# Optimization experiments

Hardware: AMD Instinct MI355X
Metric: run time of the kernel (lower is better)

The kernel has to match this reference:

```python
import jax, jax.numpy as jnp
import numpy as np

IN_FEATURES = 4096
OUT_FEATURES = 8192
LUT_SIZE = 65536  # 256 * 256 two-level codebook


def setup_inputs() -> dict:
    key = jax.random.key(0)
    k_x, k_b, k_f, k_s, k_l = jax.random.split(key, 5)
    x = jax.random.normal(k_x, (2, 256, IN_FEATURES), dtype=jnp.float32)
    base_idx = jax.random.randint(k_b, (OUT_FEATURES, IN_FEATURES), 0, 256, dtype=jnp.int32)
    fine_idx = jax.random.randint(k_f, (OUT_FEATURES, IN_FEATURES), 0, 256, dtype=jnp.int32)
    scale = jax.random.uniform(k_s, (OUT_FEATURES, 1), dtype=jnp.float32)
    lut = jax.random.normal(k_l, (LUT_SIZE,), dtype=jnp.float32)
    return {"x": x, "base_idx": base_idx, "fine_idx": fine_idx, "scale": scale, "lut": lut}


def reference(x, base_idx, fine_idx, scale, lut):
    # Two-level LUT dequant: combined 16-bit index = base*256 + fine
    combined_idx = base_idx * 256 + fine_idx              # [out, in] int32
    weights = lut[combined_idx] * scale                   # [out, in] fp32, per-row scale
    # F.linear(x, weights) == x @ weights.T
    return jnp.einsum('bsi,oi->bso', x, weights)
```

## Files before the change

### kernel.cpp

```cpp
#include <hip/hip_runtime.h>

typedef unsigned short ushort_t;
typedef unsigned int   uint32;
typedef __attribute__((ext_vector_type(8)))  short short8;
typedef __attribute__((ext_vector_type(4)))  float floatx4;
typedef __attribute__((ext_vector_type(16))) float floatx16;

#define IN_F   4096
#define OUT_F  8192
#define M_TOT  512

__device__ __forceinline__ ushort_t f2bf(float f) {
    uint32 u = __builtin_bit_cast(uint32, f);
    u += 0x7FFFu + ((u >> 16) & 1u);
    return (ushort_t)(u >> 16);
}

__global__ void cvt_x_kernel(const float* __restrict__ x, ushort_t* __restrict__ xb) {
    int i = (blockIdx.x * 256 + threadIdx.x) * 8;
    float4 v0 = *(const float4*)(x + i);
    float4 v1 = *(const float4*)(x + i + 4);
    short8 s;
    s[0] = (short)f2bf(v0.x); s[1] = (short)f2bf(v0.y);
    s[2] = (short)f2bf(v0.z); s[3] = (short)f2bf(v0.w);
    s[4] = (short)f2bf(v1.x); s[5] = (short)f2bf(v1.y);
    s[6] = (short)f2bf(v1.z); s[7] = (short)f2bf(v1.w);
    *(short8*)(xb + i) = s;
}

__global__ __launch_bounds__(1024, 4)
void dequant_kernel(const int* __restrict__ base_idx, const int* __restrict__ fine_idx,
                    const float* __restrict__ lut, ushort_t* __restrict__ wq)
{
    __shared__ ushort_t sh_lut[65536];
    const int tid = threadIdx.x;
    for (int i = tid * 4; i < 65536; i += 1024 * 4) {
        float4 v = *(const float4*)(lut + i);
        sh_lut[i + 0] = f2bf(v.x);
        sh_lut[i + 1] = f2bf(v.y);
        sh_lut[i + 2] = f2bf(v.z);
        sh_lut[i + 3] = f2bf(v.w);
    }
    __syncthreads();

    const int row = blockIdx.x * 32 + (tid >> 5);
    const int k0  = (tid & 31) * 4;
    const int* bp = base_idx + (size_t)row * IN_F + k0;
    const int* fp = fine_idx + (size_t)row * IN_F + k0;
    ushort_t*  op = wq       + (size_t)row * IN_F + k0;

    int4 cb[4], cf[4];
#pragma unroll
    for (int u = 0; u < 4; ++u) {
        cb[u] = *(const int4*)(bp + u * 128);
        cf[u] = *(const int4*)(fp + u * 128);
    }
    for (int b = 0; b < 8; ++b) {
        int4 nb[4], nf[4];
        const int bn = (b + 1 < 8) ? b + 1 : b;
#pragma unroll
        for (int u = 0; u < 4; ++u) {
            nb[u] = *(const int4*)(bp + (bn * 4 + u) * 128);
            nf[u] = *(const int4*)(fp + (bn * 4 + u) * 128);
        }
#pragma unroll
        for (int u = 0; u < 4; ++u) {
            uint32 w0 = (uint32)sh_lut[(cb[u].x << 8) + cf[u].x]
                      | ((uint32)sh_lut[(cb[u].y << 8) + cf[u].y] << 16);
            uint32 w1 = (uint32)sh_lut[(cb[u].z << 8) + cf[u].z]
                      | ((uint32)sh_lut[(cb[u].w << 8) + cf[u].w] << 16);
            uint2 wv; wv.x = w0; wv.y = w1;
            *(uint2*)(op + (size_t)(b * 4 + u) * 128) = wv;
        }
#pragma unroll
        for (int u = 0; u < 4; ++u) { cb[u] = nb[u]; cf[u] = nf[u]; }
    }
}

#define BK 128
__global__ __launch_bounds__(256)
void gemm_kernel(const ushort_t* __restrict__ xb, const ushort_t* __restrict__ wq,
                 const float* __restrict__ scale, float* __restrict__ out)
{
    __shared__ ushort_t shA[128 * BK];
    __shared__ ushort_t shB[128 * BK];

    const int tid  = threadIdx.x;
    const int wave = tid >> 6;
    const int m0   = blockIdx.x * 128;
    const int n0   = blockIdx.y * 128;

    const int g = (tid & 15) ^ ((tid >> 4) & 7);
    const ushort_t* aBase = xb + (size_t)(m0 + (tid >> 4)) * IN_F + g * 8;
    const ushort_t* bBase = wq + (size_t)(n0 + (tid >> 4)) * IN_F + g * 8;
    typedef __attribute__((address_space(3))) ushort_t lds_us;
    typedef const __attribute__((address_space(1))) void gvoid;
    lds_us* sA3 = (lds_us*)shA;
    lds_us* sB3 = (lds_us*)shB;

    const int lane = tid & 63;
    const int l31  = lane & 31;
    const int lhi  = lane >> 5;
    const int qm   = wave & 1;
    const int qn   = wave >> 1;
    const int rx   = l31 & 7;

    floatx16 acc[2][2];
    const floatx16 z16 = {0.f,0.f,0.f,0.f,0.f,0.f,0.f,0.f,0.f,0.f,0.f,0.f,0.f,0.f,0.f,0.f};
    acc[0][0] = z16; acc[0][1] = z16; acc[1][0] = z16; acc[1][1] = z16;

    for (int kb = 0; kb < IN_F; kb += BK) {
#pragma unroll
        for (int i = 0; i < 8; ++i) {
            __builtin_amdgcn_global_load_lds((gvoid*)(aBase + (size_t)i * 16 * IN_F + kb),
                (__attribute__((address_space(3))) void*)(sA3 + i * 2048 + wave * 512),
                16, 0, 0);
            __builtin_amdgcn_global_load_lds((gvoid*)(bBase + (size_t)i * 16 * IN_F + kb),
                (__attribute__((address_space(3))) void*)(sB3 + i * 2048 + wave * 512),
                16, 0, 0);
        }
        __syncthreads();

#pragma unroll
        for (int ks = 0; ks < 8; ++ks) {
            const int p = ((2 * ks + lhi) ^ rx) * 8;
            short8 a0 = *(const short8*)&shA[(qm * 64 +      l31) * BK + p];
            short8 a1 = *(const short8*)&shA[(qm * 64 + 32 + l31) * BK + p];
            short8 b0 = *(const short8*)&shB[(qn * 64 +      l31) * BK + p];
            short8 b1 = *(const short8*)&shB[(qn * 64 + 32 + l31) * BK + p];
            acc[0][0] = __builtin_amdgcn_mfma_f32_32x32x16_bf16(a0, b0, acc[0][0], 0, 0, 0);
            acc[0][1] = __builtin_amdgcn_mfma_f32_32x32x16_bf16(a0, b1, acc[0][1], 0, 0, 0);
            acc[1][0] = __builtin_amdgcn_mfma_f32_32x32x16_bf16(a1, b0, acc[1][0], 0, 0, 0);
            acc[1][1] = __builtin_amdgcn_mfma_f32_32x32x16_bf16(a1, b1, acc[1][1], 0, 0, 0);
        }
        __syncthreads();
    }

#pragma unroll
    for (int nt = 0; nt < 2; ++nt) {
        const int col = n0 + qn * 64 + nt * 32 + l31;
        const float sc = scale[col];
#pragma unroll
        for (int mt = 0; mt < 2; ++mt) {
            const int rbase = m0 + qm * 64 + mt * 32 + 4 * lhi;
#pragma unroll
            for (int reg = 0; reg < 16; ++reg) {
                const int row = rbase + (reg & 3) + 8 * (reg >> 2);
                out[(size_t)row * OUT_F + col] = acc[mt][nt][reg] * sc;
            }
        }
    }
}

#define NB  32
#define FBK 128
#define WS  136
#define NITER (IN_F / FBK)
template<bool XBF16>
__global__ __launch_bounds__(1024, 4)
void ghost_kernel(const float* __restrict__ xf, const ushort_t* __restrict__ xb,
                  const int* __restrict__ base_idx, const int* __restrict__ fine_idx,
                  const float* __restrict__ scale, const float* __restrict__ lut,
                  float* __restrict__ out)
{
    __shared__ ushort_t sh_lut[65536];
    __shared__ ushort_t sh_w[2][NB * WS];
    const int tid = threadIdx.x;
    const int n0  = blockIdx.x * NB;
    for (int i = tid * 4; i < 65536; i += 1024 * 4) {
        float4 v = *(const float4*)(lut + i);
        sh_lut[i + 0] = f2bf(v.x); sh_lut[i + 1] = f2bf(v.y);
        sh_lut[i + 2] = f2bf(v.z); sh_lut[i + 3] = f2bf(v.w);
    }
    const int sn  = tid >> 5;
    const int skq = (tid & 31) * 4;
    const int* bp = base_idx + (size_t)(n0 + sn) * IN_F + skq;
    const int* fp = fine_idx + (size_t)(n0 + sn) * IN_F + skq;
    __syncthreads();
    int4 pb = *(const int4*)(bp);
    int4 pf = *(const int4*)(fp);
    {
        uint32 w0 = (uint32)sh_lut[(pb.x << 8) + pf.x] | ((uint32)sh_lut[(pb.y << 8) + pf.y] << 16);
        uint32 w1 = (uint32)sh_lut[(pb.z << 8) + pf.z] | ((uint32)sh_lut[(pb.w << 8) + pf.w] << 16);
        uint2 wv; wv.x = w0; wv.y = w1;
        *(uint2*)&sh_w[0][sn * WS + skq] = wv;
    }
    pb = *(const int4*)(bp + FBK);
    pf = *(const int4*)(fp + FBK);
    __syncthreads();
    const int lane = tid & 63;
    const int wave = tid >> 6;
    const int l16  = lane & 15;
    const int quad = lane >> 4;
    floatx4 acc[2][2];
    const floatx4 zero = {0.f, 0.f, 0.f, 0.f};
    acc[0][0] = zero; acc[0][1] = zero; acc[1][0] = zero; acc[1][1] = zero;
    const int mrow = wave * 32 + l16;
    const ushort_t* xrow  = XBF16 ? (xb + (size_t)mrow * IN_F + quad * 8) : (const ushort_t*)nullptr;
    const float*    xrowf = XBF16 ? (const float*)nullptr : (xf + (size_t)mrow * IN_F + quad * 8);
    for (int t = 0; t < NITER; ++t) {
        const int k0 = t * FBK;
        {
            uint32 w0 = (uint32)sh_lut[(pb.x << 8) + pf.x] | ((uint32)sh_lut[(pb.y << 8) + pf.y] << 16);
            uint32 w1 = (uint32)sh_lut[(pb.z << 8) + pf.z] | ((uint32)sh_lut[(pb.w << 8) + pf.w] << 16);
            uint2 wv; wv.x = w0; wv.y = w1;
            *(uint2*)&sh_w[(t + 1) & 1][sn * WS + skq] = wv;
        }
        {
            const int kk = (t + 2 < NITER ? t + 2 : NITER - 1) * FBK;
            pb = *(const int4*)(bp + kk);
            pf = *(const int4*)(fp + kk);
        }
        const ushort_t* wb = sh_w[t & 1];
#pragma unroll
        for (int ks = 0; ks < 4; ++ks) {
            const int kk = k0 + ks * 32;
            short8 b0 = *(const short8*)&wb[l16        * WS + ks * 32 + quad * 8];
            short8 b1 = *(const short8*)&wb[(16 + l16) * WS + ks * 32 + quad * 8];
            short8 a0, a1;
            if (XBF16) {
                a0 = *(const short8*)(xrow + kk);
                a1 = *(const short8*)(xrow + (size_t)16 * IN_F + kk);
            } else {
                const float* p0 = xrowf + kk;
                const float* p1 = xrowf + (size_t)16 * IN_F + kk;
                float4 u0 = *(const float4*)p0, u1 = *(const float4*)(p0 + 4);
                float4 v0 = *(const float4*)p1, v1 = *(const float4*)(p1 + 4);
                a0[0] = (short)f2bf(u0.x); a0[1] = (short)f2bf(u0.y);
                a0[2] = (short)f2bf(u0.z); a0[3] = (short)f2bf(u0.w);
                a0[4] = (short)f2bf(u1.x); a0[5] = (short)f2bf(u1.y);
                a0[6] = (short)f2bf(u1.z); a0[7] = (short)f2bf(u1.w);
                a1[0] = (short)f2bf(v0.x); a1[1] = (short)f2bf(v0.y);
                a1[2] = (short)f2bf(v0.z); a1[3] = (short)f2bf(v0.w);
                a1[4] = (short)f2bf(v1.x); a1[5] = (short)f2bf(v1.y);
                a1[6] = (short)f2bf(v1.z); a1[7] = (short)f2bf(v1.w);
            }
            acc[0][0] = __builtin_amdgcn_mfma_f32_16x16x32_bf16(a0, b0, acc[0][0], 0, 0, 0);
            acc[0][1] = __builtin_amdgcn_mfma_f32_16x16x32_bf16(a0, b1, acc[0][1], 0, 0, 0);
            acc[1][0] = __builtin_amdgcn_mfma_f32_16x16x32_bf16(a1, b0, acc[1][0], 0, 0, 0);
            acc[1][1] = __builtin_amdgcn_mfma_f32_16x16x32_bf16(a1, b1, acc[1][1], 0, 0, 0);
        }
        __syncthreads();
    }
#pragma unroll
    for (int nf = 0; nf < 2; ++nf) {
        const int col = n0 + nf * 16 + l16;
        const float sc = scale[col];
#pragma unroll
        for (int f = 0; f < 2; ++f) {
            const int r0 = wave * 32 + f * 16 + quad * 4;
#pragma unroll
            for (int r = 0; r < 4; ++r) {
                out[(size_t)(r0 + r) * OUT_F + col] = acc[f][nf][r] * sc;
            }
        }
    }
}

extern "C" void kernel_launch(void* const* d_in, const int* in_sizes, int n_in,
                              void* d_out, int out_size, void* d_ws, size_t ws_size,
                              hipStream_t stream) {
    const float* x      = (const float*)d_in[0];
    const int*   bidx   = (const int*)d_in[1];
    const int*   fidx   = (const int*)d_in[2];
    const float* scale  = (const float*)d_in[3];
    const float* lut    = (const float*)d_in[4];
    float*       out    = (float*)d_out;

    const size_t xb_bytes = (size_t)M_TOT * IN_F * sizeof(ushort_t);
    const size_t wq_bytes = (size_t)OUT_F * IN_F * sizeof(ushort_t);

    if (ws_size >= xb_bytes + wq_bytes) {
        ushort_t* xbuf = (ushort_t*)d_ws;
        ushort_t* wbuf = (ushort_t*)((char*)d_ws + xb_bytes);
        cvt_x_kernel<<<1024, 256, 0, stream>>>(x, xbuf);
        dequant_kernel<<<256, 1024, 0, stream>>>(bidx, fidx, lut, wbuf);
        gemm_kernel<<<dim3(4, 64), 256, 0, stream>>>(xbuf, wbuf, scale, out);
    } else if (ws_size >= xb_bytes) {
        ushort_t* xbuf = (ushort_t*)d_ws;
        cvt_x_kernel<<<1024, 256, 0, stream>>>(x, xbuf);
        ghost_kernel<true><<<OUT_F / NB, 1024, 0, stream>>>(x, xbuf, bidx, fidx, scale, lut, out);
    } else {
        ghost_kernel<false><<<OUT_F / NB, 1024, 0, stream>>>(x, nullptr, bidx, fidx, scale, lut, out);
    }
}
```

Baseline: 384.2 us.

## Double-buffer GEMM LDS tiles and split dequant rows across two blocks

The GEMM now uses two LDS buffers, so the next K tile is fetched with global_load_lds while the current one feeds the MFMAs, dropping one barrier per iteration. The dequant kernel splits each row's K range across two blocks, which doubles the grid. It also issues the first index loads before the LUT-build barrier and packs the LUT writes into 32-bit stores. In exchange, LDS use in the GEMM doubles and every dequant block rebuilds the full LUT, so LUT conversion work doubles.

```diff
diff --git a/kernel.cpp b/kernel.cpp
--- a/kernel.cpp
+++ b/kernel.cpp
@@ -14,6 +14,9 @@
     uint32 u = __builtin_bit_cast(uint32, f);
     u += 0x7FFFu + ((u >> 16) & 1u);
     return (ushort_t)(u >> 16);
+}
+__device__ __forceinline__ uint32 pack2bf(float a, float b) {
+    return (uint32)f2bf(a) | ((uint32)f2bf(b) << 16);
 }
 
 __global__ void cvt_x_kernel(const float* __restrict__ x, ushort_t* __restrict__ xb) {
@@ -36,44 +39,48 @@
     const int tid = threadIdx.x;
     for (int i = tid * 4; i < 65536; i += 1024 * 4) {
         float4 v = *(const float4*)(lut + i);
-        sh_lut[i + 0] = f2bf(v.x);
-        sh_lut[i + 1] = f2bf(v.y);
-        sh_lut[i + 2] = f2bf(v.z);
-        sh_lut[i + 3] = f2bf(v.w);
+        *(uint32*)&sh_lut[i]     = pack2bf(v.x, v.y);
+        *(uint32*)&sh_lut[i + 2] = pack2bf(v.z, v.w);
+    }
+
+    const int row   = blockIdx.x * 32 + (tid >> 5);
+    const int kbase = blockIdx.y * 2048 + (tid & 31) * 4;
+    const int* bp = base_idx + (size_t)row * IN_F + kbase;
+    const int* fp = fine_idx + (size_t)row * IN_F + kbase;
+    ushort_t*  op = wq       + (size_t)row * IN_F + kbase;
+
+    int4 cb[2][4], cf[2][4];
+#pragma unroll
+    for (int u = 0; u < 4; ++u) {
+        cb[0][u] = *(const int4*)(bp + u * 128);
+        cf[0][u] = *(const int4*)(fp + u * 128);
+    }
+#pragma unroll
+    for (int u = 0; u < 4; ++u) {
+        cb[1][u] = *(const int4*)(bp + (4 + u) * 128);
+        cf[1][u] = *(const int4*)(fp + (4 + u) * 128);
     }
     __syncthreads();
 
-    const int row = blockIdx.x * 32 + (tid >> 5);
-    const int k0  = (tid & 31) * 4;
-    const int* bp = base_idx + (size_t)row * IN_F + k0;
-    const int* fp = fine_idx + (size_t)row * IN_F + k0;
-    ushort_t*  op = wq       + (size_t)row * IN_F + k0;
-
-    int4 cb[4], cf[4];
-#pragma unroll
-    for (int u = 0; u < 4; ++u) {
-        cb[u] = *(const int4*)(bp + u * 128);
-        cf[u] = *(const int4*)(fp + u * 128);
-    }
-    for (int b = 0; b < 8; ++b) {
-        int4 nb[4], nf[4];
-        const int bn = (b + 1 < 8) ? b + 1 : b;
+#pragma unroll
+    for (int b = 0; b < 4; ++b) {
+        const int cur = b & 1;
 #pragma unroll
         for (int u = 0; u < 4; ++u) {
-            nb[u] = *(const int4*)(bp + (bn * 4 + u) * 128);
-            nf[u] = *(const int4*)(fp + (bn * 4 + u) * 128);
-        }
-#pragma unroll
-        for (int u = 0; u < 4; ++u) {
-            uint32 w0 = (uint32)sh_lut[(cb[u].x << 8) + cf[u].x]
-                      | ((uint32)sh_lut[(cb[u].y << 8) + cf[u].y] << 16);
-            uint32 w1 = (uint32)sh_lut[(cb[u].z << 8) + cf[u].z]
-                      | ((uint32)sh_lut[(cb[u].w << 8) + cf[u].w] << 16);
+            uint32 w0 = (uint32)sh_lut[(cb[cur][u].x << 8) + cf[cur][u].x]
+                      | ((uint32)sh_lut[(cb[cur][u].y << 8) + cf[cur][u].y] << 16);
+            uint32 w1 = (uint32)sh_lut[(cb[cur][u].z << 8) + cf[cur][u].z]
+                      | ((uint32)sh_lut[(cb[cur][u].w << 8) + cf[cur][u].w] << 16);
             uint2 wv; wv.x = w0; wv.y = w1;
             *(uint2*)(op + (size_t)(b * 4 + u) * 128) = wv;
         }
-#pragma unroll
-        for (int u = 0; u < 4; ++u) { cb[u] = nb[u]; cf[u] = nf[u]; }
+        if (b + 2 < 4) {
+#pragma unroll
+            for (int u = 0; u < 4; ++u) {
+                cb[cur][u] = *(const int4*)(bp + ((b + 2) * 4 + u) * 128);
+                cf[cur][u] = *(const int4*)(fp + ((b + 2) * 4 + u) * 128);
+            }
+        }
     }
 }
 
@@ -82,8 +89,8 @@
 void gemm_kernel(const ushort_t* __restrict__ xb, const ushort_t* __restrict__ wq,
                  const float* __restrict__ scale, float* __restrict__ out)
 {
-    __shared__ ushort_t shA[128 * BK];
-    __shared__ ushort_t shB[128 * BK];
+    __shared__ ushort_t shA[2][128 * BK];
+    __shared__ ushort_t shB[2][128 * BK];
 
     const int tid  = threadIdx.x;
     const int wave = tid >> 6;
@@ -95,8 +102,8 @@
     const ushort_t* bBase = wq + (size_t)(n0 + (tid >> 4)) * IN_F + g * 8;
     typedef __attribute__((address_space(3))) ushort_t lds_us;
     typedef const __attribute__((address_space(1))) void gvoid;
-    lds_us* sA3 = (lds_us*)shA;
-    lds_us* sB3 = (lds_us*)shB;
+    lds_us* sA3 = (lds_us*)&shA[0][0];
+    lds_us* sB3 = (lds_us*)&shB[0][0];
 
     const int lane = tid & 63;
     const int l31  = lane & 31;
@@ -109,31 +116,46 @@
     const floatx16 z16 = {0.f,0.f,0.f,0.f,0.f,0.f,0.f,0.f,0.f,0.f,0.f,0.f,0.f,0.f,0.f,0.f};
     acc[0][0] = z16; acc[0][1] = z16; acc[1][0] = z16; acc[1][1] = z16;
 
-    for (int kb = 0; kb < IN_F; kb += BK) {
-#pragma unroll
-        for (int i = 0; i < 8; ++i) {
-            __builtin_amdgcn_global_load_lds((gvoid*)(aBase + (size_t)i * 16 * IN_F + kb),
-                (__attribute__((address_space(3))) void*)(sA3 + i * 2048 + wave * 512),
-                16, 0, 0);
-            __builtin_amdgcn_global_load_lds((gvoid*)(bBase + (size_t)i * 16 * IN_F + kb),
-                (__attribute__((address_space(3))) void*)(sB3 + i * 2048 + wave * 512),
-                16, 0, 0);
-        }
+#pragma unroll
+    for (int i = 0; i < 8; ++i) {
+        __builtin_amdgcn_global_load_lds((gvoid*)(aBase + (size_t)i * 16 * IN_F),
+            (__attribute__((address_space(3))) void*)(sA3 + i * 2048 + wave * 512), 16, 0, 0);
+        __builtin_amdgcn_global_load_lds((gvoid*)(bBase + (size_t)i * 16 * IN_F),
+            (__attribute__((address_space(3))) void*)(sB3 + i * 2048 + wave * 512), 16, 0, 0);
+    }
+
+    const int NIT = IN_F / BK;
+    for (int t = 0; t < NIT; ++t) {
         __syncthreads();
 
+        if (t + 1 < NIT) {
+            const int buf = (t + 1) & 1;
+            const size_t kb = (size_t)(t + 1) * BK;
+#pragma unroll
+            for (int i = 0; i < 8; ++i) {
+                __builtin_amdgcn_global_load_lds((gvoid*)(aBase + (size_t)i * 16 * IN_F + kb),
+                    (__attribute__((address_space(3))) void*)(sA3 + buf * 128 * BK + i * 2048 + wave * 512),
+                    16, 0, 0);
+                __builtin_amdgcn_global_load_lds((gvoid*)(bBase + (size_t)i * 16 * IN_F + kb),
+                    (__attribute__((address_space(3))) void*)(sB3 + buf * 128 * BK + i * 2048 + wave * 512),
+                    16, 0, 0);
+            }
+        }
+
+        const ushort_t* wA = shA[t & 1];
+        const ushort_t* wB = shB[t & 1];
 #pragma unroll
         for (int ks = 0; ks < 8; ++ks) {
             const int p = ((2 * ks + lhi) ^ rx) * 8;
-            short8 a0 = *(const short8*)&shA[(qm * 64 +      l31) * BK + p];
-            short8 a1 = *(const short8*)&shA[(qm * 64 + 32 + l31) * BK + p];
-            short8 b0 = *(const short8*)&shB[(qn * 64 +      l31) * BK + p];
-            short8 b1 = *(const short8*)&shB[(qn * 64 + 32 + l31) * BK + p];
+            short8 a0 = *(const short8*)&wA[(qm * 64 +      l31) * BK + p];
+            short8 a1 = *(const short8*)&wA[(qm * 64 + 32 + l31) * BK + p];
+            short8 b0 = *(const short8*)&wB[(qn * 64 +      l31) * BK + p];
+            short8 b1 = *(const short8*)&wB[(qn * 64 + 32 + l31) * BK + p];
             acc[0][0] = __builtin_amdgcn_mfma_f32_32x32x16_bf16(a0, b0, acc[0][0], 0, 0, 0);
             acc[0][1] = __builtin_amdgcn_mfma_f32_32x32x16_bf16(a0, b1, acc[0][1], 0, 0, 0);
             acc[1][0] = __builtin_amdgcn_mfma_f32_32x32x16_bf16(a1, b0, acc[1][0], 0, 0, 0);
             acc[1][1] = __builtin_amdgcn_mfma_f32_32x32x16_bf16(a1, b1, acc[1][1], 0, 0, 0);
         }
-        __syncthreads();
     }
 
 #pragma unroll
@@ -274,7 +296,7 @@
         ushort_t* xbuf = (ushort_t*)d_ws;
         ushort_t* wbuf = (ushort_t*)((char*)d_ws + xb_bytes);
         cvt_x_kernel<<<1024, 256, 0, stream>>>(x, xbuf);
-        dequant_kernel<<<256, 1024, 0, stream>>>(bidx, fidx, lut, wbuf);
+        dequant_kernel<<<dim3(256, 2), 1024, 0, stream>>>(bidx, fidx, lut, wbuf);
         gemm_kernel<<<dim3(4, 64), 256, 0, stream>>>(xbuf, wbuf, scale, out);
     } else if (ws_size >= xb_bytes) {
         ushort_t* xbuf = (ushort_t*)d_ws;
```

Result: no change. 387.9 us (+1.0%).

## Split-K GEMM with atomics, pre-convert LUT to bf16, restructure dequant loads

Applied to the files above, without the earlier changes.

The GEMM is split four ways along K, with BK reduced to 64, giving 1024 blocks instead of 256 on a many-CU GPU. Partial sums are combined with float atomicAdd into an output that a new kernel zeroes first. The LUT is converted to bf16 once in a merged conversion kernel, so each dequant block copies 128KB of bf16 instead of converting 256KB of fp32. Dequant now issues its index loads before the barrier, writes 16-byte nontemporal stores, and uses deeper prefetch. The costs are extra atomic traffic, a zeroing pass and a non-deterministic summation order.

```diff
diff --git a/kernel.cpp b/kernel.cpp
--- a/kernel.cpp
+++ b/kernel.cpp
@@ -5,6 +5,7 @@
 typedef __attribute__((ext_vector_type(8)))  short short8;
 typedef __attribute__((ext_vector_type(4)))  float floatx4;
 typedef __attribute__((ext_vector_type(16))) float floatx16;
+typedef __attribute__((ext_vector_type(4)))  uint32 uintx4;
 
 #define IN_F   4096
 #define OUT_F  8192
@@ -15,72 +16,97 @@
     u += 0x7FFFu + ((u >> 16) & 1u);
     return (ushort_t)(u >> 16);
 }
-
-__global__ void cvt_x_kernel(const float* __restrict__ x, ushort_t* __restrict__ xb) {
-    int i = (blockIdx.x * 256 + threadIdx.x) * 8;
-    float4 v0 = *(const float4*)(x + i);
-    float4 v1 = *(const float4*)(x + i + 4);
+__device__ __forceinline__ uint32 pack2bf(float a, float b) {
+    return (uint32)f2bf(a) | ((uint32)f2bf(b) << 16);
+}
+
+__global__ void cvt_kernel(const float* __restrict__ x, ushort_t* __restrict__ xb,
+                           const float* __restrict__ lut, ushort_t* __restrict__ lutb) {
+    const int bid = blockIdx.x;
+    const float* src;
+    ushort_t* dst;
+    int i;
+    if (bid < 1024) { src = x;   dst = xb;   i = bid * 2048 + threadIdx.x * 8; }
+    else            { src = lut; dst = lutb; i = (bid - 1024) * 2048 + threadIdx.x * 8; }
+    float4 v0 = *(const float4*)(src + i);
+    float4 v1 = *(const float4*)(src + i + 4);
     short8 s;
     s[0] = (short)f2bf(v0.x); s[1] = (short)f2bf(v0.y);
     s[2] = (short)f2bf(v0.z); s[3] = (short)f2bf(v0.w);
     s[4] = (short)f2bf(v1.x); s[5] = (short)f2bf(v1.y);
     s[6] = (short)f2bf(v1.z); s[7] = (short)f2bf(v1.w);
-    *(short8*)(xb + i) = s;
-}
-
-__global__ __launch_bounds__(1024, 4)
+    *(short8*)(dst + i) = s;
+}
+
+__global__ void zero_kernel(float* __restrict__ out) {
+    const int i = (blockIdx.x * 256 + threadIdx.x) * 4;
+    float4 z; z.x = 0.f; z.y = 0.f; z.z = 0.f; z.w = 0.f;
+    *(float4*)(out + i) = z;
+}
+
+template<bool PRE>
+__global__ __launch_bounds__(1024)
 void dequant_kernel(const int* __restrict__ base_idx, const int* __restrict__ fine_idx,
-                    const float* __restrict__ lut, ushort_t* __restrict__ wq)
+                    const void* __restrict__ lut_src, ushort_t* __restrict__ wq)
 {
     __shared__ ushort_t sh_lut[65536];
     const int tid = threadIdx.x;
-    for (int i = tid * 4; i < 65536; i += 1024 * 4) {
-        float4 v = *(const float4*)(lut + i);
-        sh_lut[i + 0] = f2bf(v.x);
-        sh_lut[i + 1] = f2bf(v.y);
-        sh_lut[i + 2] = f2bf(v.z);
-        sh_lut[i + 3] = f2bf(v.w);
+    if (PRE) {
+        const ushort_t* lb = (const ushort_t*)lut_src;
+#pragma unroll
+        for (int i = 0; i < 8; ++i) {
+            const int o = (tid + i * 1024) * 8;
+            *(short8*)&sh_lut[o] = *(const short8*)(lb + o);
+        }
+    } else {
+        const float* lf = (const float*)lut_src;
+        for (int i = tid * 4; i < 65536; i += 1024 * 4) {
+            float4 v = *(const float4*)(lf + i);
+            *(uint32*)&sh_lut[i]     = pack2bf(v.x, v.y);
+            *(uint32*)&sh_lut[i + 2] = pack2bf(v.z, v.w);
+        }
+    }
+
+    const int row = blockIdx.x * 32 + (tid >> 5);
+    const int kq  = (tid & 31) * 8;
+    const int* bp = base_idx + (size_t)row * IN_F + kq;
+    const int* fp = fine_idx + (size_t)row * IN_F + kq;
+    ushort_t*  op = wq       + (size_t)row * IN_F + kq;
+
+    int4 rb[4][2], rf[4][2];
+#pragma unroll
+    for (int c = 0; c < 4; ++c) {
+        rb[c][0] = *(const int4*)(bp + c * 256);
+        rb[c][1] = *(const int4*)(bp + c * 256 + 4);
+        rf[c][0] = *(const int4*)(fp + c * 256);
+        rf[c][1] = *(const int4*)(fp + c * 256 + 4);
     }
     __syncthreads();
 
-    const int row = blockIdx.x * 32 + (tid >> 5);
-    const int k0  = (tid & 31) * 4;
-    const int* bp = base_idx + (size_t)row * IN_F + k0;
-    const int* fp = fine_idx + (size_t)row * IN_F + k0;
-    ushort_t*  op = wq       + (size_t)row * IN_F + k0;
-
-    int4 cb[4], cf[4];
-#pragma unroll
-    for (int u = 0; u < 4; ++u) {
-        cb[u] = *(const int4*)(bp + u * 128);
-        cf[u] = *(const int4*)(fp + u * 128);
-    }
-    for (int b = 0; b < 8; ++b) {
-        int4 nb[4], nf[4];
-        const int bn = (b + 1 < 8) ? b + 1 : b;
-#pragma unroll
-        for (int u = 0; u < 4; ++u) {
-            nb[u] = *(const int4*)(bp + (bn * 4 + u) * 128);
-            nf[u] = *(const int4*)(fp + (bn * 4 + u) * 128);
-        }
-#pragma unroll
-        for (int u = 0; u < 4; ++u) {
-            uint32 w0 = (uint32)sh_lut[(cb[u].x << 8) + cf[u].x]
-                      | ((uint32)sh_lut[(cb[u].y << 8) + cf[u].y] << 16);
-            uint32 w1 = (uint32)sh_lut[(cb[u].z << 8) + cf[u].z]
-                      | ((uint32)sh_lut[(cb[u].w << 8) + cf[u].w] << 16);
-            uint2 wv; wv.x = w0; wv.y = w1;
-            *(uint2*)(op + (size_t)(b * 4 + u) * 128) = wv;
-        }
-#pragma unroll
-        for (int u = 0; u < 4; ++u) { cb[u] = nb[u]; cf[u] = nf[u]; }
-    }
-}
-
-#define BK 128
-__global__ __launch_bounds__(256)
-void gemm_kernel(const ushort_t* __restrict__ xb, const ushort_t* __restrict__ wq,
-                 const float* __restrict__ scale, float* __restrict__ out)
+#pragma unroll
+    for (int c = 0; c < 16; ++c) {
+        const int s = c & 3;
+        const int4 b0 = rb[s][0], b1 = rb[s][1];
+        const int4 f0 = rf[s][0], f1 = rf[s][1];
+        if (c + 4 < 16) {
+            rb[s][0] = *(const int4*)(bp + (c + 4) * 256);
+            rb[s][1] = *(const int4*)(bp + (c + 4) * 256 + 4);
+            rf[s][0] = *(const int4*)(fp + (c + 4) * 256);
+            rf[s][1] = *(const int4*)(fp + (c + 4) * 256 + 4);
+        }
+        uintx4 wv;
+        wv.x = (uint32)sh_lut[(b0.x << 8) + f0.x] | ((uint32)sh_lut[(b0.y << 8) + f0.y] << 16);
+        wv.y = (uint32)sh_lut[(b0.z << 8) + f0.z] | ((uint32)sh_lut[(b0.w << 8) + f0.w] << 16);
+        wv.z = (uint32)sh_lut[(b1.x << 8) + f1.x] | ((uint32)sh_lut[(b1.y << 8) + f1.y] << 16);
+        wv.w = (uint32)sh_lut[(b1.z << 8) + f1.z] | ((uint32)sh_lut[(b1.w << 8) + f1.w] << 16);
+        __builtin_nontemporal_store(wv, (uintx4*)(op + (size_t)c * 256));
+    }
+}
+
+#define BK 64
+__global__ __launch_bounds__(256, 4)
+void gemm_split4_kernel(const ushort_t* __restrict__ xb, const ushort_t* __restrict__ wq,
+                        const float* __restrict__ scale, float* __restrict__ out)
 {
     __shared__ ushort_t shA[128 * BK];
     __shared__ ushort_t shB[128 * BK];
@@ -89,10 +115,11 @@
     const int wave = tid >> 6;
     const int m0   = blockIdx.x * 128;
     const int n0   = blockIdx.y * 128;
-
-    const int g = (tid & 15) ^ ((tid >> 4) & 7);
-    const ushort_t* aBase = xb + (size_t)(m0 + (tid >> 4)) * IN_F + g * 8;
-    const ushort_t* bBase = wq + (size_t)(n0 + (tid >> 4)) * IN_F + g * 8;
+    const int kz   = blockIdx.z * (IN_F / 4);
+
+    const int g = (tid & 7) ^ ((tid >> 3) & 7);
+    const ushort_t* aBase = xb + (size_t)(m0 + (tid >> 3)) * IN_F + kz + g * 8;
+    const ushort_t* bBase = wq + (size_t)(n0 + (tid >> 3)) * IN_F + kz + g * 8;
     typedef __attribute__((address_space(3))) ushort_t lds_us;
     typedef const __attribute__((address_space(1))) void gvoid;
     lds_us* sA3 = (lds_us*)shA;
@@ -109,20 +136,20 @@
     const floatx16 z16 = {0.f,0.f,0.f,0.f,0.f,0.f,0.f,0.f,0.f,0.f,0.f,0.f,0.f,0.f,0.f,0.f};
     acc[0][0] = z16; acc[0][1] = z16; acc[1][0] = z16; acc[1][1] = z16;
 
-    for (int kb = 0; kb < IN_F; kb += BK) {
-#pragma unroll
-        for (int i = 0; i < 8; ++i) {
-            __builtin_amdgcn_global_load_lds((gvoid*)(aBase + (size_t)i * 16 * IN_F + kb),
+    for (int kb = 0; kb < IN_F / 4; kb += BK) {
+#pragma unroll
+        for (int i = 0; i < 4; ++i) {
+            __builtin_amdgcn_global_load_lds((gvoid*)(aBase + (size_t)i * 32 * IN_F + kb),
                 (__attribute__((address_space(3))) void*)(sA3 + i * 2048 + wave * 512),
                 16, 0, 0);
-            __builtin_amdgcn_global_load_lds((gvoid*)(bBase + (size_t)i * 16 * IN_F + kb),
+            __builtin_amdgcn_global_load_lds((gvoid*)(bBase + (size_t)i * 32 * IN_F + kb),
                 (__attribute__((address_space(3))) void*)(sB3 + i * 2048 + wave * 512),
                 16, 0, 0);
         }
         __syncthreads();
 
 #pragma unroll
-        for (int ks = 0; ks < 8; ++ks) {
+        for (int ks = 0; ks < 4; ++ks) {
             const int p = ((2 * ks + lhi) ^ rx) * 8;
             short8 a0 = *(const short8*)&shA[(qm * 64 +      l31) * BK + p];
             short8 a1 = *(const short8*)&shA[(qm * 64 + 32 + l31) * BK + p];
@@ -146,7 +173,7 @@
 #pragma unroll
             for (int reg = 0; reg < 16; ++reg) {
                 const int row = rbase + (reg & 3) + 8 * (reg >> 2);
-                out[(size_t)row * OUT_F + col] = acc[mt][nt][reg] * sc;
+                atomicAdd(&out[(size_t)row * OUT_F + col], acc[mt][nt][reg] * sc);
             }
         }
     }
@@ -267,18 +294,28 @@
     const float* lut    = (const float*)d_in[4];
     float*       out    = (float*)d_out;
 
-    const size_t xb_bytes = (size_t)M_TOT * IN_F * sizeof(ushort_t);
-    const size_t wq_bytes = (size_t)OUT_F * IN_F * sizeof(ushort_t);
-
-    if (ws_size >= xb_bytes + wq_bytes) {
+    const size_t xb_bytes  = (size_t)M_TOT * IN_F * sizeof(ushort_t);
+    const size_t wq_bytes  = (size_t)OUT_F * IN_F * sizeof(ushort_t);
+    const size_t lut_bytes = (size_t)65536 * sizeof(ushort_t);
+
+    if (ws_size >= xb_bytes + wq_bytes + lut_bytes) {
         ushort_t* xbuf = (ushort_t*)d_ws;
         ushort_t* wbuf = (ushort_t*)((char*)d_ws + xb_bytes);
-        cvt_x_kernel<<<1024, 256, 0, stream>>>(x, xbuf);
-        dequant_kernel<<<256, 1024, 0, stream>>>(bidx, fidx, lut, wbuf);
-        gemm_kernel<<<dim3(4, 64), 256, 0, stream>>>(xbuf, wbuf, scale, out);
+        ushort_t* lbuf = (ushort_t*)((char*)d_ws + xb_bytes + wq_bytes);
+        zero_kernel<<<(M_TOT * OUT_F) / (256 * 4), 256, 0, stream>>>(out);
+        cvt_kernel<<<1056, 256, 0, stream>>>(x, xbuf, lut, lbuf);
+        dequant_kernel<true><<<OUT_F / 32, 1024, 0, stream>>>(bidx, fidx, lbuf, wbuf);
+        gemm_split4_kernel<<<dim3(4, 64, 4), 256, 0, stream>>>(xbuf, wbuf, scale, out);
+    } else if (ws_size >= xb_bytes + wq_bytes) {
+        ushort_t* xbuf = (ushort_t*)d_ws;
+        ushort_t* wbuf = (ushort_t*)((char*)d_ws + xb_bytes);
+        zero_kernel<<<(M_TOT * OUT_F) / (256 * 4), 256, 0, stream>>>(out);
+        cvt_kernel<<<1024, 256, 0, stream>>>(x, xbuf, lut, nullptr);
+        dequant_kernel<false><<<OUT_F / 32, 1024, 0, stream>>>(bidx, fidx, lut, wbuf);
+        gemm_split4_kernel<<<dim3(4, 64, 4), 256, 0, stream>>>(xbuf, wbuf, scale, out);
     } else if (ws_size >= xb_bytes) {
         ushort_t* xbuf = (ushort_t*)d_ws;
-        cvt_x_kernel<<<1024, 256, 0, stream>>>(x, xbuf);
+        cvt_kernel<<<1024, 256, 0, stream>>>(x, xbuf, lut, nullptr);
         ghost_kernel<true><<<OUT_F / NB, 1024, 0, stream>>>(x, xbuf, bidx, fidx, scale, lut, out);
     } else {
         ghost_kernel<false><<<OUT_F / NB, 1024, 0, stream>>>(x, nullptr, bidx, fidx, scale, lut, out);
```

After: 393.7 us. 2.5% more time.
